# Kernel optimization log

Measured on AMD Instinct MI355X. Metric: run time of the kernel, lower is better.

## Reference

```python
import jax, jax.numpy as jnp
import numpy as np

B, NPG, EPG = 128, 256, 2048   # graphs, nodes/graph, edges/graph
EMB, EH, L = 256, 64, 5
ATOM_V, BOND_V = 119, 16


def setup_inputs() -> dict:
    key = jax.random.key(0)
    ks = iter(jax.random.split(key, 32))
    s = 0.02
    inp = {
        'atom_idx': jax.random.randint(next(ks), (B, NPG), 0, ATOM_V),
        'local_edge_index': jax.random.randint(next(ks), (B, 2, EPG), 0, NPG),
        'edge_attr_idx': jax.random.randint(next(ks), (B, EPG), 0, BOND_V),
        'order': 3,
        'atom_emb': jax.random.normal(next(ks), (ATOM_V, EMB), jnp.float32) * s,
        'bond_emb_h': jax.random.normal(next(ks), (BOND_V, EH), jnp.float32) * s,
        'edge_lin_w': jax.random.normal(next(ks), (EH,), jnp.float32) * s,
        'edge_lin_b': jax.random.normal(next(ks), (1,), jnp.float32) * s,
        'bond_emb_l': jax.random.normal(next(ks), (L, BOND_V, EMB), jnp.float32) * s,
        'gin_eps': jnp.zeros((L,), jnp.float32),
        'mlp_w1': jax.random.normal(next(ks), (L, EMB, 2 * EMB), jnp.float32) * s,
        'mlp_b1': jax.random.normal(next(ks), (L, 2 * EMB), jnp.float32) * s,
        'mlp_bn_g': jnp.ones((L, 2 * EMB), jnp.float32),
        'mlp_bn_b': jnp.zeros((L, 2 * EMB), jnp.float32),
        'mlp_w2': jax.random.normal(next(ks), (L, 2 * EMB, EMB), jnp.float32) * s,
        'mlp_b2': jax.random.normal(next(ks), (L, EMB), jnp.float32) * s,
        'out_bn_g': jnp.ones((L, EMB), jnp.float32),
        'out_bn_b': jnp.zeros((L, EMB), jnp.float32),
        'vn_emb': jnp.zeros((1, EMB), jnp.float32),  # init constant 0 as in source
        'vn_w1': jax.random.normal(next(ks), (L - 1, EMB, 2 * EMB), jnp.float32) * s,
        'vn_b1': jax.random.normal(next(ks), (L - 1, 2 * EMB), jnp.float32) * s,
        'vn_w2': jax.random.normal(next(ks), (L - 1, 2 * EMB, EMB), jnp.float32) * s,
        'vn_b2': jax.random.normal(next(ks), (L - 1, EMB), jnp.float32) * s,
    }
    return inp


def _batchnorm(x, g, b):
    # training-mode BN math (biased variance), eps=1e-5 as in torch.nn.BatchNorm1d
    mu = x.mean(0)
    var = ((x - mu) ** 2).mean(0)
    return (x - mu) * jax.lax.rsqrt(var + 1e-5) * g + b


def reference(atom_idx, local_edge_index, edge_attr_idx, order,
              atom_emb, bond_emb_h, edge_lin_w, edge_lin_b, bond_emb_l, gin_eps,
              mlp_w1, mlp_b1, mlp_bn_g, mlp_bn_b, mlp_w2, mlp_b2,
              out_bn_g, out_bn_b, vn_emb, vn_w1, vn_b1, vn_w2, vn_b2):
    Bg, n = atom_idx.shape
    emb = atom_emb.shape[1]
    N = Bg * n
    nl = gin_eps.shape[0]

    # ---- per-graph learned-adjacency dense propagation (adj_learn=1) ----
    fea = atom_emb[atom_idx]                                       # [B,n,emb]
    ew = jax.nn.sigmoid(jnp.einsum('beh,h->be', bond_emb_h[edge_attr_idx], edge_lin_w)
                        + edge_lin_b[0])                           # [B,e]

    def per_graph(f, ei, w):
        adj = jnp.zeros((n, n), f.dtype).at[ei[0], ei[1]].set(w)
        adj = adj + jnp.eye(n, dtype=f.dtype)
        # A = diag(colsum^-1/2) @ adj @ diag(rowsum^-1/2)  (as in source naming)
        r_row = adj.sum(0) ** -0.5
        r_col = adj.sum(1) ** -0.5
        A = r_row[:, None] * adj * r_col[None, :]
        x = f
        y = f
        for _ in range(order):
            x = A @ x
            y = y + x
        return y / (order + 1.0)

    h = jax.vmap(per_graph)(fea, local_edge_index, ew).reshape(N, emb)

    # ---- flatten batched graph to global edge list ----
    batch = jnp.repeat(jnp.arange(Bg), n)                          # [N]
    off = (jnp.arange(Bg) * n)[:, None]
    src = (local_edge_index[:, 0] + off).reshape(-1)               # [E]
    dst = (local_edge_index[:, 1] + off).reshape(-1)
    ea = edge_attr_idx.reshape(-1)

    # ---- virtual-node GIN stack (eval: dropout = identity) ----
    vn = jnp.broadcast_to(vn_emb[0], (Bg, emb))
    for l in range(nl):
        h = h + vn[batch]
        h_in = h
        eemb = bond_emb_l[l][ea]                                   # [E,emb]
        msg = jax.nn.relu(h[src] + eemb)
        agg = jax.ops.segment_sum(msg, dst, num_segments=N)
        z = (1.0 + gin_eps[l]) * h + agg
        z = _batchnorm(z @ mlp_w1[l] + mlp_b1[l], mlp_bn_g[l], mlp_bn_b[l])
        z = jax.nn.relu(z) @ mlp_w2[l] + mlp_b2[l]
        z = _batchnorm(z, out_bn_g[l], out_bn_b[l])
        if l < nl - 1:
            z = jax.nn.relu(z)
            vt = jax.ops.segment_sum(h_in, batch, num_segments=Bg) + vn
            vn = jax.nn.relu(jax.nn.relu(vt @ vn_w1[l] + vn_b1[l]) @ vn_w2[l] + vn_b2[l])
        h = z
    return h  # JK='last'
```

## Files before the change

kernel.cpp:

```cpp
#include <hip/hip_runtime.h>
#include <math.h>


#define B_G   128
#define NPG   256
#define EPG   2048
#define EMB   256
#define NL    5
#define NNODE (B_G*NPG)
#define NEDGE (B_G*EPG)
#define FBUF  8388608

typedef __attribute__((ext_vector_type(8))) short bf16x8;
typedef __attribute__((ext_vector_type(4))) float f32x4;

__device__ __forceinline__ void split1(float x, unsigned short& h, unsigned short& l) {
  unsigned u = __builtin_bit_cast(unsigned, x);
  unsigned hr = u + 0x7FFFu + ((u >> 16) & 1u);
  h = (unsigned short)(hr >> 16);
  float hf = __builtin_bit_cast(float, hr & 0xFFFF0000u);
  float r = x - hf;
  unsigned v = __builtin_bit_cast(unsigned, r);
  unsigned lr = v + 0x7FFFu + ((v >> 16) & 1u);
  l = (unsigned short)(lr >> 16);
}

__device__ __forceinline__ unsigned short round1(float x) {
  unsigned u = __builtin_bit_cast(unsigned, x);
  return (unsigned short)((u + 0x7FFFu + ((u >> 16) & 1u)) >> 16);
}

__device__ __forceinline__ float bdec(unsigned short h) {
  return __builtin_bit_cast(float, (unsigned)h << 16);
}

__device__ __forceinline__ void gload16(unsigned short* lds, const unsigned short* g) {
  __builtin_amdgcn_global_load_lds(
      (const __attribute__((address_space(1))) unsigned int*)g,
      (__attribute__((address_space(3))) unsigned int*)lds, 16, 0, 0);
}

__global__ void k_zero(uint4* p, int n16) {
  int i = blockIdx.x * 256 + threadIdx.x;
  if (i < n16) p[i] = make_uint4(0, 0, 0, 0);
}

__global__ void k_ewtbl(const float* __restrict__ bh, const float* __restrict__ w,
                        const float* __restrict__ b, float* __restrict__ tbl) {
  int v = threadIdx.x >> 6, t = threadIdx.x & 63;
  float p = bh[v * 64 + t] * w[t];
  for (int off = 32; off; off >>= 1) p += __shfl_down(p, off, 64);
  if (t == 0) tbl[v] = 1.0f / (1.0f + expf(-(p + b[0])));
}

__global__ void k_pack_adj(const int* __restrict__ lei, const int* __restrict__ ea,
                           int* __restrict__ packed) {
  int idx = blockIdx.x * 256 + threadIdx.x;
  int g = idx >> 11, e = idx & 2047;
  int s = lei[g * 4096 + e];
  int d = lei[g * 4096 + 2048 + e];
  int v = ((e + 1) << 4) | ea[g * 2048 + e];
  atomicMax(&packed[g * 65536 + s * 256 + d], v);
}

__global__ void k_unpack_adj(const int* __restrict__ packed,
                             const float* __restrict__ tbl, float* __restrict__ adj) {
  int idx = blockIdx.x * 256 + threadIdx.x;
  int v = packed[idx];
  adj[idx] = v ? tbl[v & 15] : 0.0f;
}

__global__ void k_addeye(float* __restrict__ adj) {
  int idx = blockIdx.x * 256 + threadIdx.x;
  int g = idx >> 8, i = idx & 255;
  adj[g * 65536 + i * 257] += 1.0f;
}

__global__ __launch_bounds__(256)
void k_degnorm(float* __restrict__ adj) {
  int g = blockIdx.x, t = threadIdx.x;
  float* Ag = adj + (size_t)g * 65536;
  __shared__ float cs[256];
  float s0 = 0, s1 = 0, s2 = 0, s3 = 0;
  for (int i = 0; i < 256; i += 4) {
    s0 += Ag[(i + 0) * 256 + t]; s1 += Ag[(i + 1) * 256 + t];
    s2 += Ag[(i + 2) * 256 + t]; s3 += Ag[(i + 3) * 256 + t];
  }
  cs[t] = rsqrtf((s0 + s1) + (s2 + s3));
  float4 r0 = make_float4(0, 0, 0, 0), r1 = r0, r2 = r0, r3 = r0;
  const float4* A4 = (const float4*)(Ag + t * 256);
  for (int j = 0; j < 64; j += 4) {
    float4 v0 = A4[j], v1 = A4[j + 1], v2 = A4[j + 2], v3 = A4[j + 3];
    r0.x += v0.x + v0.y; r0.y += v0.z + v0.w;
    r1.x += v1.x + v1.y; r1.y += v1.z + v1.w;
    r2.x += v2.x + v2.y; r2.y += v2.z + v2.w;
    r3.x += v3.x + v3.y; r3.y += v3.z + v3.w;
  }
  float rc = rsqrtf((r0.x + r0.y) + (r1.x + r1.y) + (r2.x + r2.y) + (r3.x + r3.y));
  __syncthreads();
  for (int i = 0; i < 256; i++) Ag[i * 256 + t] = cs[i] * Ag[i * 256 + t] * rc;
}

__global__ void k_feaT(const int* __restrict__ aidx, const float* __restrict__ aemb,
                       float* __restrict__ X0t, float* __restrict__ Yt) {
  int i = blockIdx.x * 256 + threadIdx.x;
  int g = i >> 16, e = (i >> 8) & 255, n = i & 255;
  int av = aidx[g * 256 + n];
  float v = aemb[av * 256 + e];
  X0t[i] = v; Yt[i] = v;
}

__global__ __launch_bounds__(256)
void k_transp(const float* __restrict__ src, float* __restrict__ dst,
              int K, int N, long ss, long sd, float scale) {
  __shared__ float tl[64][65];
  src += (size_t)blockIdx.z * ss; dst += (size_t)blockIdx.z * sd;
  int n0 = blockIdx.x * 64, k0 = blockIdx.y * 64;
  int t = threadIdx.x;
  int c = (t & 15) * 4, r = t >> 4;
#pragma unroll
  for (int p = 0; p < 4; p++) {
    int rr = r + p * 16;
    float4 v = *(const float4*)&src[(size_t)(k0 + rr) * N + n0 + c];
    tl[rr][c] = v.x; tl[rr][c + 1] = v.y; tl[rr][c + 2] = v.z; tl[rr][c + 3] = v.w;
  }
  __syncthreads();
#pragma unroll
  for (int p = 0; p < 4; p++) {
    int rr = r + p * 16;
    float4 o;
    o.x = tl[c][rr] * scale;     o.y = tl[c + 1][rr] * scale;
    o.z = tl[c + 2][rr] * scale; o.w = tl[c + 3][rr] * scale;
    *(float4*)&dst[(size_t)(n0 + rr) * K + k0 + c] = o;
  }
}

__global__ __launch_bounds__(256)
void k_wtsplit(const float* __restrict__ src, unsigned short* __restrict__ dh,
               unsigned short* __restrict__ dl, int K, int N, long ss, long sd) {
  __shared__ float tl[64][65];
  src += (size_t)blockIdx.z * ss;
  dh += (size_t)blockIdx.z * sd; dl += (size_t)blockIdx.z * sd;
  int n0 = blockIdx.x * 64, k0 = blockIdx.y * 64;
  int t = threadIdx.x;
  int c = (t & 15) * 4, r = t >> 4;
#pragma unroll
  for (int p = 0; p < 4; p++) {
    int rr = r + p * 16;
    float4 v = *(const float4*)&src[(size_t)(k0 + rr) * N + n0 + c];
    tl[rr][c] = v.x; tl[rr][c + 1] = v.y; tl[rr][c + 2] = v.z; tl[rr][c + 3] = v.w;
  }
  __syncthreads();
#pragma unroll
  for (int p = 0; p < 4; p++) {
    int rr = r + p * 16;
    ushort4 hh, ll;
    split1(tl[c][rr],     hh.x, ll.x);
    split1(tl[c + 1][rr], hh.y, ll.y);
    split1(tl[c + 2][rr], hh.z, ll.z);
    split1(tl[c + 3][rr], hh.w, ll.w);
    size_t o = (size_t)(n0 + rr) * K + k0 + c;
    *(ushort4*)&dh[o] = hh; *(ushort4*)&dl[o] = ll;
  }
}

__global__ __launch_bounds__(256, 2)
void k_mgemm(const float* __restrict__ A, const float* __restrict__ Bt,
             float* __restrict__ C, float* __restrict__ Yacc, int K, int N,
             long sA, long sBt, long sC) {
  __shared__ alignas(16) unsigned short Ah[128 * 64], Al[128 * 64];
  __shared__ alignas(16) unsigned short Bh[128 * 64], Bl[128 * 64];
  int z = blockIdx.z;
  A += (size_t)z * sA; Bt += (size_t)z * sBt; C += (size_t)z * sC;
  float* Yp = Yacc ? Yacc + (size_t)z * sC : nullptr;
  int rowbase = blockIdx.y * 128, colbase = blockIdx.x * 128;
  int t = threadIdx.x, l = t & 63, w = t >> 6;
  int wr = w >> 1, wc = w & 1;
  f32x4 acc[4][4];
#pragma unroll
  for (int i = 0; i < 4; i++)
#pragma unroll
    for (int j = 0; j < 4; j++) acc[i][j] = (f32x4){0, 0, 0, 0};

  for (int k0 = 0; k0 < K; k0 += 64) {
    __syncthreads();
    for (int p = 0; p < 8; p++) {
      int flat = p * 256 + t;
      int r = flat >> 4, kq = (flat & 15) * 4;
      float4 va = *(const float4*)&A[(size_t)(rowbase + r) * K + k0 + kq];
      int off = ((r * 128 + kq * 2) ^ ((r & 7) << 4)) >> 1;
      ushort4 hh, ll;
      split1(va.x, hh.x, ll.x); split1(va.y, hh.y, ll.y);
      split1(va.z, hh.z, ll.z); split1(va.w, hh.w, ll.w);
      *(ushort4*)&Ah[off] = hh; *(ushort4*)&Al[off] = ll;
      float4 vb = *(const float4*)&Bt[(size_t)(colbase + r) * K + k0 + kq];
      split1(vb.x, hh.x, ll.x); split1(vb.y, hh.y, ll.y);
      split1(vb.z, hh.z, ll.z); split1(vb.w, hh.w, ll.w);
      *(ushort4*)&Bh[off] = hh; *(ushort4*)&Bl[off] = ll;
    }
    __syncthreads();
#pragma unroll
    for (int ks = 0; ks < 2; ks++) {
      bf16x8 ah[4], al_[4], bh[4], bl[4];
#pragma unroll
      for (int fm = 0; fm < 4; fm++) {
        int r = wr * 64 + fm * 16 + (l & 15);
        int off = (r * 64 + ks * 32 + (l >> 4) * 8) ^ ((r & 7) << 3);
        ah[fm] = *(const bf16x8*)&Ah[off];
        al_[fm] = *(const bf16x8*)&Al[off];
      }
#pragma unroll
      for (int fn = 0; fn < 4; fn++) {
        int c = wc * 64 + fn * 16 + (l & 15);
        int off = (c * 64 + ks * 32 + (l >> 4) * 8) ^ ((c & 7) << 3);
        bh[fn] = *(const bf16x8*)&Bh[off];
        bl[fn] = *(const bf16x8*)&Bl[off];
      }
#pragma unroll
      for (int fm = 0; fm < 4; fm++)
#pragma unroll
        for (int fn = 0; fn < 4; fn++) {
          acc[fm][fn] = __builtin_amdgcn_mfma_f32_16x16x32_bf16(ah[fm], bh[fn], acc[fm][fn], 0, 0, 0);
          acc[fm][fn] = __builtin_amdgcn_mfma_f32_16x16x32_bf16(ah[fm], bl[fn], acc[fm][fn], 0, 0, 0);
          acc[fm][fn] = __builtin_amdgcn_mfma_f32_16x16x32_bf16(al_[fm], bh[fn], acc[fm][fn], 0, 0, 0);
        }
    }
  }
#pragma unroll
  for (int fm = 0; fm < 4; fm++)
#pragma unroll
    for (int r4 = 0; r4 < 4; r4++) {
      int row = rowbase + wr * 64 + fm * 16 + (l >> 4) * 4 + r4;
#pragma unroll
      for (int fn = 0; fn < 4; fn++) {
        int col = colbase + wc * 64 + fn * 16 + (l & 15);
        float v = acc[fm][fn][r4];
        size_t idx = (size_t)row * N + col;
        if (Yp) Yp[idx] += v;
        C[idx] = v;
      }
    }
}

__global__ __launch_bounds__(256, 4)
void k_bgemm(const unsigned short* __restrict__ A_g, const unsigned short* __restrict__ B_g,
             const float* __restrict__ bias, float* __restrict__ Cf,
             unsigned short* __restrict__ Ch,
             float* __restrict__ Ssum, float* __restrict__ Ssq, int K, int N) {
  __shared__ alignas(16) unsigned short As[128 * 64];
  __shared__ alignas(16) unsigned short Bs[128 * 64];
  int rowbase = blockIdx.y * 128, colbase = blockIdx.x * 128;
  int t = threadIdx.x, l = t & 63, wid = t >> 6;
  int wr = wid >> 1, wc = wid & 1;
  int r8 = l >> 3, cb = (l & 7) * 8;
  f32x4 acc[4][4];
#pragma unroll
  for (int i = 0; i < 4; i++)
#pragma unroll
    for (int j = 0; j < 4; j++) acc[i][j] = (f32x4){0, 0, 0, 0};

  for (int k0 = 0; k0 < K; k0 += 64) {
    __syncthreads();
#pragma unroll
    for (int i = 0; i < 4; i++) {
      int chunk = wid * 4 + i;
      int row = chunk * 8 + r8;
      gload16(As + chunk * 512, A_g + (size_t)(rowbase + row) * K + k0 + cb);
      gload16(Bs + chunk * 512, B_g + (size_t)(colbase + row) * K + k0 + cb);
    }
    __syncthreads();
#pragma unroll
    for (int ks = 0; ks < 2; ks++) {
      bf16x8 ah[4], bh[4];
#pragma unroll
      for (int fm = 0; fm < 4; fm++) {
        int r = wr * 64 + fm * 16 + (l & 15);
        ah[fm] = *(const bf16x8*)&As[r * 64 + ks * 32 + (l >> 4) * 8];
      }
#pragma unroll
      for (int fn = 0; fn < 4; fn++) {
        int c = wc * 64 + fn * 16 + (l & 15);
        bh[fn] = *(const bf16x8*)&Bs[c * 64 + ks * 32 + (l >> 4) * 8];
      }
#pragma unroll
      for (int fm = 0; fm < 4; fm++)
#pragma unroll
        for (int fn = 0; fn < 4; fn++)
          acc[fm][fn] = __builtin_amdgcn_mfma_f32_16x16x32_bf16(ah[fm], bh[fn], acc[fm][fn], 0, 0, 0);
    }
  }
  __syncthreads();
  float bi[4], scoll[4] = {0, 0, 0, 0}, qcoll[4] = {0, 0, 0, 0};
#pragma unroll
  for (int fn = 0; fn < 4; fn++)
    bi[fn] = bias ? bias[colbase + wc * 64 + fn * 16 + (l & 15)] : 0.0f;
#pragma unroll
  for (int fm = 0; fm < 4; fm++)
#pragma unroll
    for (int r4 = 0; r4 < 4; r4++) {
      int row = rowbase + wr * 64 + fm * 16 + (l >> 4) * 4 + r4;
#pragma unroll
      for (int fn = 0; fn < 4; fn++) {
        int col = colbase + wc * 64 + fn * 16 + (l & 15);
        float v = acc[fm][fn][r4] + bi[fn];
        size_t idx = (size_t)row * N + col;
        if (Cf) Cf[idx] = v;
        if (Ch) Ch[idx] = round1(v);
        scoll[fn] += v; qcoll[fn] += v * v;
      }
    }
  if (Ssum) {
    float* scr = (float*)As;
    scr[t] = 0.0f;
    __syncthreads();
#pragma unroll
    for (int fn = 0; fn < 4; fn++) {
      int cl_ = wc * 64 + fn * 16 + (l & 15);
      atomicAdd(&scr[cl_ * 2], scoll[fn]);
      atomicAdd(&scr[cl_ * 2 + 1], qcoll[fn]);
    }
    __syncthreads();
    if (t < 128) {
      atomicAdd(&Ssum[colbase + t], scr[t * 2]);
      atomicAdd(&Ssq[colbase + t], scr[t * 2 + 1]);
    }
  }
}

__global__ void k_bnsplit(unsigned short* __restrict__ Th,
                          const float* __restrict__ Ssum, const float* __restrict__ Ssq,
                          const float* __restrict__ g, const float* __restrict__ b) {
  size_t i = (size_t)blockIdx.x * 256 + threadIdx.x;
  int c4 = ((int)i & 127) * 4;
  ushort4 h4 = *(ushort4*)&Th[i * 4];
  float4 ss = *(const float4*)&Ssum[c4], qq = *(const float4*)&Ssq[c4];
  float4 gg = *(const float4*)&g[c4],    bb = *(const float4*)&b[c4];
  const float invN = 1.0f / 32768.0f;
  float x, mu, var, sc, sh;
#define BNS(cmp) \
  mu = ss.cmp * invN; var = qq.cmp * invN - mu * mu; \
  sc = rsqrtf(var + 1e-5f) * gg.cmp; sh = bb.cmp - mu * sc; \
  x = bdec(h4.cmp); x = fmaf(x, sc, sh); x = x > 0 ? x : 0; \
  h4.cmp = round1(x);
  BNS(x) BNS(y) BNS(z) BNS(w)
#undef BNS
  *(ushort4*)&Th[i * 4] = h4;
}

__global__ void k_count(const int* __restrict__ lei, int* __restrict__ counts) {
  int idx = blockIdx.x * 256 + threadIdx.x;
  int g = idx >> 11, e = idx & 2047;
  int d = lei[g * 4096 + 2048 + e];
  atomicAdd(&counts[g * 256 + d], 1);
}

__global__ void k_scan(const int* __restrict__ counts, int* __restrict__ rowptr,
                       int* __restrict__ pos) {
  int g = blockIdx.x, t = threadIdx.x;
  __shared__ int sc[256];
  int own = counts[g * 256 + t];
  sc[t] = own;
  __syncthreads();
  for (int off = 1; off < 256; off <<= 1) {
    int v = 0;
    if (t >= off) v = sc[t - off];
    __syncthreads();
    sc[t] += v;
    __syncthreads();
  }
  int val = g * 2048 + sc[t] - own;
  rowptr[g * 256 + t] = val;
  pos[g * 256 + t] = val;
  if (g == B_G - 1 && t == 255) rowptr[B_G * 256] = B_G * 2048;
}

__global__ void k_fill(const int* __restrict__ lei, const int* __restrict__ ea,
                       int* __restrict__ pos, int* __restrict__ csr) {
  int idx = blockIdx.x * 256 + threadIdx.x;
  int g = idx >> 11, e = idx & 2047;
  int s = lei[g * 4096 + e];
  int d = lei[g * 4096 + 2048 + e];
  int eav = ea[g * 2048 + e];
  int slot = atomicAdd(&pos[g * 256 + d], 1);
  csr[slot] = s | (eav << 16);
}

__global__ __launch_bounds__(256)
void k_agg(const float* __restrict__ H,
           const float* __restrict__ hsc, const float* __restrict__ hsh,
           const float* __restrict__ vn, int vns,
           const float* __restrict__ eemb,
           const int* __restrict__ rowptr, const int* __restrict__ csr,
           const float* __restrict__ geps, int l,
           unsigned short* __restrict__ Zh) {
  __shared__ float ee[16 * 256];
  for (int i = threadIdx.x; i < 4096; i += 256) ee[i] = eemb[i];
  __syncthreads();
  int lane = threadIdx.x & 63, w = threadIdx.x >> 6;
  int m = blockIdx.x * 4 + w;
  int g = m >> 8;
  int d = lane * 4;
  float eps1 = 1.0f + geps[l];
  float4 sc4 = make_float4(0, 0, 0, 0), sh4 = make_float4(0, 0, 0, 0);
  if (hsc) { sc4 = *(const float4*)&hsc[d]; sh4 = *(const float4*)&hsh[d]; }
  float4 vn4 = *(const float4*)&vn[(size_t)g * vns + d];
  int rp = rowptr[m], rp1 = rowptr[m + 1];
  float4 acc = make_float4(0, 0, 0, 0);
  int gbase = g << 8;
  for (int j = rp; j < rp1; j++) {
    int cw = csr[j];
    int src = cw & 0xFFFF, eav = cw >> 16;
    float4 h4 = *(const float4*)&H[(size_t)(gbase + src) * 256 + d];
    if (hsc) {
      h4.x = fmaf(h4.x, sc4.x, sh4.x); h4.y = fmaf(h4.y, sc4.y, sh4.y);
      h4.z = fmaf(h4.z, sc4.z, sh4.z); h4.w = fmaf(h4.w, sc4.w, sh4.w);
      h4.x = h4.x > 0 ? h4.x : 0; h4.y = h4.y > 0 ? h4.y : 0;
      h4.z = h4.z > 0 ? h4.z : 0; h4.w = h4.w > 0 ? h4.w : 0;
    }
    const float4 e4 = *(const float4*)&ee[eav * 256 + d];
    float mx = h4.x + vn4.x + e4.x; float my = h4.y + vn4.y + e4.y;
    float mz = h4.z + vn4.z + e4.z; float mw = h4.w + vn4.w + e4.w;
    acc.x += mx > 0 ? mx : 0; acc.y += my > 0 ? my : 0;
    acc.z += mz > 0 ? mz : 0; acc.w += mw > 0 ? mw : 0;
  }
  float4 hs = *(const float4*)&H[(size_t)m * 256 + d];
  if (hsc) {
    hs.x = fmaf(hs.x, sc4.x, sh4.x); hs.y = fmaf(hs.y, sc4.y, sh4.y);
    hs.z = fmaf(hs.z, sc4.z, sh4.z); hs.w = fmaf(hs.w, sc4.w, sh4.w);
    hs.x = hs.x > 0 ? hs.x : 0; hs.y = hs.y > 0 ? hs.y : 0;
    hs.z = hs.z > 0 ? hs.z : 0; hs.w = hs.w > 0 ? hs.w : 0;
  }
  float4 z4;
  z4.x = eps1 * (hs.x + vn4.x) + acc.x;
  z4.y = eps1 * (hs.y + vn4.y) + acc.y;
  z4.z = eps1 * (hs.z + vn4.z) + acc.z;
  z4.w = eps1 * (hs.w + vn4.w) + acc.w;
  ushort4 hh;
  hh.x = round1(z4.x); hh.y = round1(z4.y);
  hh.z = round1(z4.z); hh.w = round1(z4.w);
  *(ushort4*)&Zh[(size_t)m * 256 + d] = hh;
}

__global__ __launch_bounds__(256)
void k_vnsum(const float* __restrict__ H,
             const float* __restrict__ hsc, const float* __restrict__ hsh,
             float* __restrict__ VNP) {
  int g = blockIdx.x >> 1, p = blockIdx.x & 1, t = threadIdx.x;
  float sc = 0, sh = 0;
  if (hsc) { sc = hsc[t]; sh = hsh[t]; }
  int base = g * 256 + p * 128;
  float s0 = 0, s1 = 0, s2 = 0, s3 = 0;
  for (int i = 0; i < 128; i += 4) {
    float v0 = H[(size_t)(base + i + 0) * 256 + t];
    float v1 = H[(size_t)(base + i + 1) * 256 + t];
    float v2 = H[(size_t)(base + i + 2) * 256 + t];
    float v3 = H[(size_t)(base + i + 3) * 256 + t];
    if (hsc) {
      v0 = fmaf(v0, sc, sh); v0 = v0 > 0 ? v0 : 0;
      v1 = fmaf(v1, sc, sh); v1 = v1 > 0 ? v1 : 0;
      v2 = fmaf(v2, sc, sh); v2 = v2 > 0 ? v2 : 0;
      v3 = fmaf(v3, sc, sh); v3 = v3 > 0 ? v3 : 0;
    }
    s0 += v0; s1 += v1; s2 += v2; s3 += v3;
  }
  VNP[(size_t)(p * 128 + g) * 256 + t] = (s0 + s1) + (s2 + s3);
}

__global__ __launch_bounds__(256)
void k_vn(const float* __restrict__ VNP,
          const float* __restrict__ vn_in, int vns,
          const float* __restrict__ W1, const float* __restrict__ B1,
          const float* __restrict__ W2, const float* __restrict__ B2,
          float* __restrict__ vn_out) {
  int g = blockIdx.x, t = threadIdx.x;
  __shared__ float vt[256];
  __shared__ float u[512];
  vt[t] = VNP[(size_t)g * 256 + t] + VNP[(size_t)(128 + g) * 256 + t]
        + 257.0f * vn_in[(size_t)g * vns + t];
  __syncthreads();
  for (int o = t; o < 512; o += 256) {
    float a = B1[o];
    for (int k = 0; k < 256; k++) a = fmaf(vt[k], W1[k * 512 + o], a);
    u[o] = a > 0 ? a : 0;
  }
  __syncthreads();
  float a = B2[t];
  for (int k = 0; k < 512; k++) a = fmaf(u[k], W2[k * 256 + t], a);
  vn_out[g * 256 + t] = a > 0 ? a : 0;
}

__global__ void k_bnfin(const float* __restrict__ Ssum, const float* __restrict__ Ssq,
                        const float* __restrict__ g, const float* __restrict__ b,
                        float* __restrict__ scale, float* __restrict__ shift,
                        int NC, float invN) {
  int c = blockIdx.x * 256 + threadIdx.x;
  if (c >= NC) return;
  float mu = Ssum[c] * invN;
  float var = Ssq[c] * invN - mu * mu;
  float rs = rsqrtf(var + 1e-5f);
  float s = rs * g[c];
  scale[c] = s;
  shift[c] = b[c] - mu * s;
}

__global__ void k_final(const float* __restrict__ T2, const float* __restrict__ sc,
                        const float* __restrict__ sh, float* __restrict__ out) {
  int i = blockIdx.x * 256 + threadIdx.x;
  int c4 = (i & 63) * 4;
  float4 v = *(const float4*)&T2[(size_t)i * 4];
  float4 s4 = *(const float4*)&sc[c4];
  float4 h4 = *(const float4*)&sh[c4];
  v.x = fmaf(v.x, s4.x, h4.x); v.y = fmaf(v.y, s4.y, h4.y);
  v.z = fmaf(v.z, s4.z, h4.z); v.w = fmaf(v.w, s4.w, h4.w);
  *(float4*)&out[(size_t)i * 4] = v;
}

extern "C" void kernel_launch(void* const* d_in, const int* in_sizes, int n_in,
                              void* d_out, int out_size, void* d_ws, size_t ws_size,
                              hipStream_t stream) {
  (void)in_sizes; (void)n_in; (void)out_size; (void)ws_size;
  const int*   atom_idx = (const int*)d_in[0];
  const int*   lei      = (const int*)d_in[1];
  const int*   eattr    = (const int*)d_in[2];
  const float* atom_emb = (const float*)d_in[4];
  const float* bemb_h   = (const float*)d_in[5];
  const float* elw      = (const float*)d_in[6];
  const float* elb      = (const float*)d_in[7];
  const float* bemb_l   = (const float*)d_in[8];
  const float* geps     = (const float*)d_in[9];
  const float* mw1      = (const float*)d_in[10];
  const float* mb1      = (const float*)d_in[11];
  const float* mbng     = (const float*)d_in[12];
  const float* mbnb     = (const float*)d_in[13];
  const float* mw2      = (const float*)d_in[14];
  const float* mb2      = (const float*)d_in[15];
  const float* obng     = (const float*)d_in[16];
  const float* obnb     = (const float*)d_in[17];
  const float* vne      = (const float*)d_in[18];
  const float* vw1      = (const float*)d_in[19];
  const float* vb1      = (const float*)d_in[20];
  const float* vw2      = (const float*)d_in[21];
  const float* vb2      = (const float*)d_in[22];
  float* out = (float*)d_out;

  float* W   = (float*)d_ws;
  float* A_  = W;
  float* X0T = W + (size_t)FBUF;
  float* X1T = W + (size_t)2 * FBUF;
  float* YT  = W + (size_t)3 * FBUF;
  float* Z_  = W + (size_t)4 * FBUF;
  float* SM  = W + (size_t)5 * FBUF;
  float* EWT = SM;
  float* S1S = SM + 256;
  float* S1Q = SM + 768;
  float* S2S = SM + 1280;
  float* S2Q = SM + 1536;
  float* SC2 = SM + 1792;
  float* SH2 = SM + 2048;
  float* VNA = SM + 2304;
  float* VNB = SM + 35072;
  int* ROWPTR = (int*)(SM + 67840);
  int* POS    = ROWPTR + 32772;
  int* COUNTS = POS + 32768;
  int* CSR    = COUNTS + 32768;
  unsigned short* W1hT = (unsigned short*)(SM + 428544);
  unsigned short* W1lT = (unsigned short*)(SM + 756224);
  unsigned short* W2hT = (unsigned short*)(SM + 1083904);
  unsigned short* W2lT = (unsigned short*)(SM + 1411584);
  float* T2 = A_;
  float* H0 = X0T;
  unsigned short* T1h = (unsigned short*)X1T;
  unsigned short* Zh  = (unsigned short*)Z_;
  int* PACKED = (int*)Z_;
  float* VNP  = (float*)POS;

  k_zero<<<8192, 256, 0, stream>>>((uint4*)A_, 2097152);
  k_zero<<<8192, 256, 0, stream>>>((uint4*)PACKED, 2097152);
  k_zero<<<32, 256, 0, stream>>>((uint4*)COUNTS, 8192);
  k_ewtbl<<<1, 1024, 0, stream>>>(bemb_h, elw, elb, EWT);
  k_pack_adj<<<NEDGE / 256, 256, 0, stream>>>(lei, eattr, PACKED);
  k_unpack_adj<<<32768, 256, 0, stream>>>(PACKED, EWT, A_);
  k_addeye<<<NNODE / 256, 256, 0, stream>>>(A_);
  k_degnorm<<<B_G, 256, 0, stream>>>(A_);
  k_wtsplit<<<dim3(8, 4, 5), 256, 0, stream>>>(mw1, W1hT, W1lT, 256, 512, 131072, 131072);
  k_wtsplit<<<dim3(4, 8, 5), 256, 0, stream>>>(mw2, W2hT, W2lT, 512, 256, 131072, 131072);
  k_feaT<<<32768, 256, 0, stream>>>(atom_idx, atom_emb, X0T, YT);
  k_mgemm<<<dim3(2, 2, B_G), 256, 0, stream>>>(X0T, A_, X1T, YT, 256, 256, 65536, 65536, 65536);
  k_mgemm<<<dim3(2, 2, B_G), 256, 0, stream>>>(X1T, A_, X0T, YT, 256, 256, 65536, 65536, 65536);
  k_mgemm<<<dim3(2, 2, B_G), 256, 0, stream>>>(X0T, A_, X1T, YT, 256, 256, 65536, 65536, 65536);
  k_transp<<<dim3(4, 4, B_G), 256, 0, stream>>>(YT, H0, 256, 256, 65536, 65536, 0.25f);

  k_count<<<NEDGE / 256, 256, 0, stream>>>(lei, COUNTS);
  k_scan<<<B_G, 256, 0, stream>>>(COUNTS, ROWPTR, POS);
  k_fill<<<NEDGE / 256, 256, 0, stream>>>(lei, eattr, POS, CSR);

  const float* vn_cur = vne; int vns = 0;
  float* vn_next = VNA;
  for (int l = 0; l < NL; l++) {
    const float* hsrc = (l == 0) ? H0 : T2;
    const float* hsc  = (l == 0) ? nullptr : SC2;
    const float* hsh  = (l == 0) ? nullptr : SH2;
    k_agg<<<NNODE / 4, 256, 0, stream>>>(hsrc, hsc, hsh, vn_cur, vns,
        bemb_l + (size_t)l * 16 * EMB, ROWPTR, CSR, geps, l, Zh);
    if (l < NL - 1) {
      k_vnsum<<<256, 256, 0, stream>>>(hsrc, hsc, hsh, VNP);
      k_vn<<<B_G, 256, 0, stream>>>(VNP, vn_cur, vns,
          vw1 + (size_t)l * EMB * 512, vb1 + (size_t)l * 512,
          vw2 + (size_t)l * 512 * EMB, vb2 + (size_t)l * EMB, vn_next);
    }
    k_zero<<<2, 256, 0, stream>>>((uint4*)S1S, 384);
    k_bgemm<<<dim3(4, 256), 256, 0, stream>>>(Zh,
        W1hT + (size_t)l * 131072, mb1 + (size_t)l * 512,
        nullptr, T1h, S1S, S1Q, 256, 512);
    k_bnsplit<<<16384, 256, 0, stream>>>(T1h, S1S, S1Q,
        mbng + (size_t)l * 512, mbnb + (size_t)l * 512);
    k_bgemm<<<dim3(2, 256), 256, 0, stream>>>(T1h,
        W2hT + (size_t)l * 131072, mb2 + (size_t)l * 256,
        T2, nullptr, S2S, S2Q, 512, 256);
    k_bnfin<<<1, 256, 0, stream>>>(S2S, S2Q, obng + (size_t)l * EMB,
        obnb + (size_t)l * EMB, SC2, SH2, 256, 1.0f / NNODE);
    if (l < NL - 1) {
      vn_cur = vn_next; vns = EMB;
      vn_next = (vn_next == VNA) ? VNB : VNA;
    }
  }
  k_final<<<8192, 256, 0, stream>>>(T2, SC2, SH2, out);
}
```

Measured before the change: 1.197 ms.

## Replace split-bf16 propagation GEMMs with single-bf16 batched GEMMs

```diff
diff --git a/kernel.cpp b/kernel.cpp
--- a/kernel.cpp
+++ b/kernel.cpp
@@ -14,17 +14,6 @@
 typedef __attribute__((ext_vector_type(8))) short bf16x8;
 typedef __attribute__((ext_vector_type(4))) float f32x4;
 
-__device__ __forceinline__ void split1(float x, unsigned short& h, unsigned short& l) {
-  unsigned u = __builtin_bit_cast(unsigned, x);
-  unsigned hr = u + 0x7FFFu + ((u >> 16) & 1u);
-  h = (unsigned short)(hr >> 16);
-  float hf = __builtin_bit_cast(float, hr & 0xFFFF0000u);
-  float r = x - hf;
-  unsigned v = __builtin_bit_cast(unsigned, r);
-  unsigned lr = v + 0x7FFFu + ((v >> 16) & 1u);
-  l = (unsigned short)(lr >> 16);
-}
-
 __device__ __forceinline__ unsigned short round1(float x) {
   unsigned u = __builtin_bit_cast(unsigned, x);
   return (unsigned short)((u + 0x7FFFu + ((u >> 16) & 1u)) >> 16);
@@ -67,26 +56,21 @@
                              const float* __restrict__ tbl, float* __restrict__ adj) {
   int idx = blockIdx.x * 256 + threadIdx.x;
   int v = packed[idx];
-  adj[idx] = v ? tbl[v & 15] : 0.0f;
-}
-
-__global__ void k_addeye(float* __restrict__ adj) {
-  int idx = blockIdx.x * 256 + threadIdx.x;
-  int g = idx >> 8, i = idx & 255;
-  adj[g * 65536 + i * 257] += 1.0f;
+  int r = (idx >> 8) & 255, c = idx & 255;
+  adj[idx] = (v ? tbl[v & 15] : 0.0f) + (r == c ? 1.0f : 0.0f);
 }
 
 __global__ __launch_bounds__(256)
-void k_degnorm(float* __restrict__ adj) {
+void k_degsums(const float* __restrict__ adj, float* __restrict__ CSv,
+               float* __restrict__ RCv) {
   int g = blockIdx.x, t = threadIdx.x;
-  float* Ag = adj + (size_t)g * 65536;
-  __shared__ float cs[256];
+  const float* Ag = adj + (size_t)g * 65536;
   float s0 = 0, s1 = 0, s2 = 0, s3 = 0;
   for (int i = 0; i < 256; i += 4) {
     s0 += Ag[(i + 0) * 256 + t]; s1 += Ag[(i + 1) * 256 + t];
     s2 += Ag[(i + 2) * 256 + t]; s3 += Ag[(i + 3) * 256 + t];
   }
-  cs[t] = rsqrtf((s0 + s1) + (s2 + s3));
+  CSv[g * 256 + t] = rsqrtf((s0 + s1) + (s2 + s3));
   float4 r0 = make_float4(0, 0, 0, 0), r1 = r0, r2 = r0, r3 = r0;
   const float4* A4 = (const float4*)(Ag + t * 256);
   for (int j = 0; j < 64; j += 4) {
@@ -96,25 +80,77 @@
     r2.x += v2.x + v2.y; r2.y += v2.z + v2.w;
     r3.x += v3.x + v3.y; r3.y += v3.z + v3.w;
   }
-  float rc = rsqrtf((r0.x + r0.y) + (r1.x + r1.y) + (r2.x + r2.y) + (r3.x + r3.y));
-  __syncthreads();
-  for (int i = 0; i < 256; i++) Ag[i * 256 + t] = cs[i] * Ag[i * 256 + t] * rc;
-}
-
-__global__ void k_feaT(const int* __restrict__ aidx, const float* __restrict__ aemb,
-                       float* __restrict__ X0t, float* __restrict__ Yt) {
-  int i = blockIdx.x * 256 + threadIdx.x;
-  int g = i >> 16, e = (i >> 8) & 255, n = i & 255;
-  int av = aidx[g * 256 + n];
-  float v = aemb[av * 256 + e];
-  X0t[i] = v; Yt[i] = v;
+  RCv[g * 256 + t] = rsqrtf((r0.x + r0.y) + (r1.x + r1.y) + (r2.x + r2.y) + (r3.x + r3.y));
+}
+
+__global__ void k_ascale(const float* __restrict__ adj, const float* __restrict__ CSv,
+                         const float* __restrict__ RCv, unsigned short* __restrict__ Ahb) {
+  int flat = blockIdx.x * 256 + threadIdx.x;
+  int g = flat >> 14;
+  int i = (flat >> 6) & 255, j4 = (flat & 63) * 4;
+  size_t base = (size_t)g * 65536 + i * 256 + j4;
+  float4 a = *(const float4*)&adj[base];
+  float cs = CSv[g * 256 + i];
+  float4 rc = *(const float4*)&RCv[g * 256 + j4];
+  ushort4 o;
+  o.x = round1(cs * a.x * rc.x); o.y = round1(cs * a.y * rc.y);
+  o.z = round1(cs * a.z * rc.z); o.w = round1(cs * a.w * rc.w);
+  *(ushort4*)&Ahb[base] = o;
+}
+
+__global__ void k_feaTb(const int* __restrict__ aidx, const float* __restrict__ aemb,
+                        unsigned short* __restrict__ X0h) {
+  int flat = blockIdx.x * 256 + threadIdx.x;
+  int base = flat * 4;
+  int g = base >> 16, e = (base >> 8) & 255, n0 = base & 255;
+  const int* ai = &aidx[g * 256 + n0];
+  ushort4 o;
+  o.x = round1(aemb[ai[0] * 256 + e]);
+  o.y = round1(aemb[ai[1] * 256 + e]);
+  o.z = round1(aemb[ai[2] * 256 + e]);
+  o.w = round1(aemb[ai[3] * 256 + e]);
+  *(ushort4*)&X0h[base] = o;
 }
 
 __global__ __launch_bounds__(256)
-void k_transp(const float* __restrict__ src, float* __restrict__ dst,
-              int K, int N, long ss, long sd, float scale) {
+void k_sumT(const unsigned short* __restrict__ X0, const unsigned short* __restrict__ X1,
+            const unsigned short* __restrict__ X2, const unsigned short* __restrict__ X3,
+            float* __restrict__ dst) {
   __shared__ float tl[64][65];
-  src += (size_t)blockIdx.z * ss; dst += (size_t)blockIdx.z * sd;
+  size_t zo = (size_t)blockIdx.z * 65536;
+  int n0 = blockIdx.x * 64, k0 = blockIdx.y * 64;
+  int t = threadIdx.x;
+  int c = (t & 15) * 4, r = t >> 4;
+#pragma unroll
+  for (int p = 0; p < 4; p++) {
+    int rr = r + p * 16;
+    size_t off = zo + (size_t)(k0 + rr) * 256 + n0 + c;
+    ushort4 a = *(const ushort4*)&X0[off];
+    ushort4 b = *(const ushort4*)&X1[off];
+    ushort4 cc = *(const ushort4*)&X2[off];
+    ushort4 d = *(const ushort4*)&X3[off];
+    tl[rr][c + 0] = bdec(a.x) + bdec(b.x) + bdec(cc.x) + bdec(d.x);
+    tl[rr][c + 1] = bdec(a.y) + bdec(b.y) + bdec(cc.y) + bdec(d.y);
+    tl[rr][c + 2] = bdec(a.z) + bdec(b.z) + bdec(cc.z) + bdec(d.z);
+    tl[rr][c + 3] = bdec(a.w) + bdec(b.w) + bdec(cc.w) + bdec(d.w);
+  }
+  __syncthreads();
+#pragma unroll
+  for (int p = 0; p < 4; p++) {
+    int rr = r + p * 16;
+    float4 o;
+    o.x = tl[c][rr] * 0.25f;     o.y = tl[c + 1][rr] * 0.25f;
+    o.z = tl[c + 2][rr] * 0.25f; o.w = tl[c + 3][rr] * 0.25f;
+    *(float4*)&dst[zo + (size_t)(n0 + rr) * 256 + k0 + c] = o;
+  }
+}
+
+__global__ __launch_bounds__(256)
+void k_wtb(const float* __restrict__ src, unsigned short* __restrict__ dh,
+           int K, int N, long ss, long sd) {
+  __shared__ float tl[64][65];
+  src += (size_t)blockIdx.z * ss;
+  dh += (size_t)blockIdx.z * sd;
   int n0 = blockIdx.x * 64, k0 = blockIdx.y * 64;
   int t = threadIdx.x;
   int c = (t & 15) * 4, r = t >> 4;
@@ -128,127 +164,25 @@
 #pragma unroll
   for (int p = 0; p < 4; p++) {
     int rr = r + p * 16;
-    float4 o;
-    o.x = tl[c][rr] * scale;     o.y = tl[c + 1][rr] * scale;
-    o.z = tl[c + 2][rr] * scale; o.w = tl[c + 3][rr] * scale;
-    *(float4*)&dst[(size_t)(n0 + rr) * K + k0 + c] = o;
-  }
-}
-
-__global__ __launch_bounds__(256)
-void k_wtsplit(const float* __restrict__ src, unsigned short* __restrict__ dh,
-               unsigned short* __restrict__ dl, int K, int N, long ss, long sd) {
-  __shared__ float tl[64][65];
-  src += (size_t)blockIdx.z * ss;
-  dh += (size_t)blockIdx.z * sd; dl += (size_t)blockIdx.z * sd;
-  int n0 = blockIdx.x * 64, k0 = blockIdx.y * 64;
-  int t = threadIdx.x;
-  int c = (t & 15) * 4, r = t >> 4;
-#pragma unroll
-  for (int p = 0; p < 4; p++) {
-    int rr = r + p * 16;
-    float4 v = *(const float4*)&src[(size_t)(k0 + rr) * N + n0 + c];
-    tl[rr][c] = v.x; tl[rr][c + 1] = v.y; tl[rr][c + 2] = v.z; tl[rr][c + 3] = v.w;
-  }
-  __syncthreads();
-#pragma unroll
-  for (int p = 0; p < 4; p++) {
-    int rr = r + p * 16;
-    ushort4 hh, ll;
-    split1(tl[c][rr],     hh.x, ll.x);
-    split1(tl[c + 1][rr], hh.y, ll.y);
-    split1(tl[c + 2][rr], hh.z, ll.z);
-    split1(tl[c + 3][rr], hh.w, ll.w);
-    size_t o = (size_t)(n0 + rr) * K + k0 + c;
-    *(ushort4*)&dh[o] = hh; *(ushort4*)&dl[o] = ll;
-  }
-}
-
-__global__ __launch_bounds__(256, 2)
-void k_mgemm(const float* __restrict__ A, const float* __restrict__ Bt,
-             float* __restrict__ C, float* __restrict__ Yacc, int K, int N,
-             long sA, long sBt, long sC) {
-  __shared__ alignas(16) unsigned short Ah[128 * 64], Al[128 * 64];
-  __shared__ alignas(16) unsigned short Bh[128 * 64], Bl[128 * 64];
-  int z = blockIdx.z;
-  A += (size_t)z * sA; Bt += (size_t)z * sBt; C += (size_t)z * sC;
-  float* Yp = Yacc ? Yacc + (size_t)z * sC : nullptr;
-  int rowbase = blockIdx.y * 128, colbase = blockIdx.x * 128;
-  int t = threadIdx.x, l = t & 63, w = t >> 6;
-  int wr = w >> 1, wc = w & 1;
-  f32x4 acc[4][4];
-#pragma unroll
-  for (int i = 0; i < 4; i++)
-#pragma unroll
-    for (int j = 0; j < 4; j++) acc[i][j] = (f32x4){0, 0, 0, 0};
-
-  for (int k0 = 0; k0 < K; k0 += 64) {
-    __syncthreads();
-    for (int p = 0; p < 8; p++) {
-      int flat = p * 256 + t;
-      int r = flat >> 4, kq = (flat & 15) * 4;
-      float4 va = *(const float4*)&A[(size_t)(rowbase + r) * K + k0 + kq];
-      int off = ((r * 128 + kq * 2) ^ ((r & 7) << 4)) >> 1;
-      ushort4 hh, ll;
-      split1(va.x, hh.x, ll.x); split1(va.y, hh.y, ll.y);
-      split1(va.z, hh.z, ll.z); split1(va.w, hh.w, ll.w);
-      *(ushort4*)&Ah[off] = hh; *(ushort4*)&Al[off] = ll;
-      float4 vb = *(const float4*)&Bt[(size_t)(colbase + r) * K + k0 + kq];
-      split1(vb.x, hh.x, ll.x); split1(vb.y, hh.y, ll.y);
-      split1(vb.z, hh.z, ll.z); split1(vb.w, hh.w, ll.w);
-      *(ushort4*)&Bh[off] = hh; *(ushort4*)&Bl[off] = ll;
-    }
-    __syncthreads();
-#pragma unroll
-    for (int ks = 0; ks < 2; ks++) {
-      bf16x8 ah[4], al_[4], bh[4], bl[4];
-#pragma unroll
-      for (int fm = 0; fm < 4; fm++) {
-        int r = wr * 64 + fm * 16 + (l & 15);
-        int off = (r * 64 + ks * 32 + (l >> 4) * 8) ^ ((r & 7) << 3);
-        ah[fm] = *(const bf16x8*)&Ah[off];
-        al_[fm] = *(const bf16x8*)&Al[off];
-      }
-#pragma unroll
-      for (int fn = 0; fn < 4; fn++) {
-        int c = wc * 64 + fn * 16 + (l & 15);
-        int off = (c * 64 + ks * 32 + (l >> 4) * 8) ^ ((c & 7) << 3);
-        bh[fn] = *(const bf16x8*)&Bh[off];
-        bl[fn] = *(const bf16x8*)&Bl[off];
-      }
-#pragma unroll
-      for (int fm = 0; fm < 4; fm++)
-#pragma unroll
-        for (int fn = 0; fn < 4; fn++) {
-          acc[fm][fn] = __builtin_amdgcn_mfma_f32_16x16x32_bf16(ah[fm], bh[fn], acc[fm][fn], 0, 0, 0);
-          acc[fm][fn] = __builtin_amdgcn_mfma_f32_16x16x32_bf16(ah[fm], bl[fn], acc[fm][fn], 0, 0, 0);
-          acc[fm][fn] = __builtin_amdgcn_mfma_f32_16x16x32_bf16(al_[fm], bh[fn], acc[fm][fn], 0, 0, 0);
-        }
-    }
-  }
-#pragma unroll
-  for (int fm = 0; fm < 4; fm++)
-#pragma unroll
-    for (int r4 = 0; r4 < 4; r4++) {
-      int row = rowbase + wr * 64 + fm * 16 + (l >> 4) * 4 + r4;
-#pragma unroll
-      for (int fn = 0; fn < 4; fn++) {
-        int col = colbase + wc * 64 + fn * 16 + (l & 15);
-        float v = acc[fm][fn][r4];
-        size_t idx = (size_t)row * N + col;
-        if (Yp) Yp[idx] += v;
-        C[idx] = v;
-      }
-    }
+    ushort4 hh;
+    hh.x = round1(tl[c][rr]);     hh.y = round1(tl[c + 1][rr]);
+    hh.z = round1(tl[c + 2][rr]); hh.w = round1(tl[c + 3][rr]);
+    *(ushort4*)&dh[(size_t)(n0 + rr) * K + k0 + c] = hh;
+  }
 }
 
 __global__ __launch_bounds__(256, 4)
 void k_bgemm(const unsigned short* __restrict__ A_g, const unsigned short* __restrict__ B_g,
              const float* __restrict__ bias, float* __restrict__ Cf,
              unsigned short* __restrict__ Ch,
-             float* __restrict__ Ssum, float* __restrict__ Ssq, int K, int N) {
+             float* __restrict__ Ssum, float* __restrict__ Ssq, int K, int N,
+             long zA, long zB, long zC) {
   __shared__ alignas(16) unsigned short As[128 * 64];
   __shared__ alignas(16) unsigned short Bs[128 * 64];
+  int z = blockIdx.z;
+  A_g += (size_t)z * zA; B_g += (size_t)z * zB;
+  if (Cf) Cf += (size_t)z * zC;
+  if (Ch) Ch += (size_t)z * zC;
   int rowbase = blockIdx.y * 128, colbase = blockIdx.x * 128;
   int t = threadIdx.x, l = t & 63, wid = t >> 6;
   int wr = wid >> 1, wc = wid & 1;
@@ -545,9 +479,9 @@
 
   float* W   = (float*)d_ws;
   float* A_  = W;
-  float* X0T = W + (size_t)FBUF;
-  float* X1T = W + (size_t)2 * FBUF;
-  float* YT  = W + (size_t)3 * FBUF;
+  float* U1  = W + (size_t)FBUF;
+  float* U2  = W + (size_t)2 * FBUF;
+  float* U3  = W + (size_t)3 * FBUF;
   float* Z_  = W + (size_t)4 * FBUF;
   float* SM  = W + (size_t)5 * FBUF;
   float* EWT = SM;
@@ -559,36 +493,43 @@
   float* SH2 = SM + 2048;
   float* VNA = SM + 2304;
   float* VNB = SM + 35072;
-  int* ROWPTR = (int*)(SM + 67840);
+  float* CSv = SM + 67840;
+  float* RCv = SM + 100608;
+  int* ROWPTR = (int*)(SM + 133376);
   int* POS    = ROWPTR + 32772;
   int* COUNTS = POS + 32768;
   int* CSR    = COUNTS + 32768;
-  unsigned short* W1hT = (unsigned short*)(SM + 428544);
-  unsigned short* W1lT = (unsigned short*)(SM + 756224);
-  unsigned short* W2hT = (unsigned short*)(SM + 1083904);
-  unsigned short* W2lT = (unsigned short*)(SM + 1411584);
+  unsigned short* W1hT = (unsigned short*)(SM + 493952);
+  unsigned short* W2hT = (unsigned short*)(SM + 821632);
   float* T2 = A_;
-  float* H0 = X0T;
-  unsigned short* T1h = (unsigned short*)X1T;
+  float* H0 = U3;
+  int* PACKED = (int*)U3;
+  unsigned short* X0h = (unsigned short*)U1;
+  unsigned short* X1h = X0h + 8388608;
+  unsigned short* X2h = (unsigned short*)U2;
+  unsigned short* X3h = X2h + 8388608;
+  unsigned short* T1h = (unsigned short*)U1;
   unsigned short* Zh  = (unsigned short*)Z_;
-  int* PACKED = (int*)Z_;
+  unsigned short* Ahb = (unsigned short*)(Z_ + (size_t)FBUF / 2);
   float* VNP  = (float*)POS;
 
-  k_zero<<<8192, 256, 0, stream>>>((uint4*)A_, 2097152);
   k_zero<<<8192, 256, 0, stream>>>((uint4*)PACKED, 2097152);
   k_zero<<<32, 256, 0, stream>>>((uint4*)COUNTS, 8192);
   k_ewtbl<<<1, 1024, 0, stream>>>(bemb_h, elw, elb, EWT);
   k_pack_adj<<<NEDGE / 256, 256, 0, stream>>>(lei, eattr, PACKED);
   k_unpack_adj<<<32768, 256, 0, stream>>>(PACKED, EWT, A_);
-  k_addeye<<<NNODE / 256, 256, 0, stream>>>(A_);
-  k_degnorm<<<B_G, 256, 0, stream>>>(A_);
-  k_wtsplit<<<dim3(8, 4, 5), 256, 0, stream>>>(mw1, W1hT, W1lT, 256, 512, 131072, 131072);
-  k_wtsplit<<<dim3(4, 8, 5), 256, 0, stream>>>(mw2, W2hT, W2lT, 512, 256, 131072, 131072);
-  k_feaT<<<32768, 256, 0, stream>>>(atom_idx, atom_emb, X0T, YT);
-  k_mgemm<<<dim3(2, 2, B_G), 256, 0, stream>>>(X0T, A_, X1T, YT, 256, 256, 65536, 65536, 65536);
-  k_mgemm<<<dim3(2, 2, B_G), 256, 0, stream>>>(X1T, A_, X0T, YT, 256, 256, 65536, 65536, 65536);
-  k_mgemm<<<dim3(2, 2, B_G), 256, 0, stream>>>(X0T, A_, X1T, YT, 256, 256, 65536, 65536, 65536);
-  k_transp<<<dim3(4, 4, B_G), 256, 0, stream>>>(YT, H0, 256, 256, 65536, 65536, 0.25f);
+  k_degsums<<<B_G, 256, 0, stream>>>(A_, CSv, RCv);
+  k_ascale<<<8192, 256, 0, stream>>>(A_, CSv, RCv, Ahb);
+  k_wtb<<<dim3(8, 4, 5), 256, 0, stream>>>(mw1, W1hT, 256, 512, 131072, 131072);
+  k_wtb<<<dim3(4, 8, 5), 256, 0, stream>>>(mw2, W2hT, 512, 256, 131072, 131072);
+  k_feaTb<<<8192, 256, 0, stream>>>(atom_idx, atom_emb, X0h);
+  k_bgemm<<<dim3(2, 2, B_G), 256, 0, stream>>>(X0h, Ahb, nullptr, nullptr, X1h,
+      nullptr, nullptr, 256, 256, 65536, 65536, 65536);
+  k_bgemm<<<dim3(2, 2, B_G), 256, 0, stream>>>(X1h, Ahb, nullptr, nullptr, X2h,
+      nullptr, nullptr, 256, 256, 65536, 65536, 65536);
+  k_bgemm<<<dim3(2, 2, B_G), 256, 0, stream>>>(X2h, Ahb, nullptr, nullptr, X3h,
+      nullptr, nullptr, 256, 256, 65536, 65536, 65536);
+  k_sumT<<<dim3(4, 4, B_G), 256, 0, stream>>>(X0h, X1h, X2h, X3h, H0);
 
   k_count<<<NEDGE / 256, 256, 0, stream>>>(lei, COUNTS);
   k_scan<<<B_G, 256, 0, stream>>>(COUNTS, ROWPTR, POS);
@@ -609,14 +550,14 @@
           vw2 + (size_t)l * 512 * EMB, vb2 + (size_t)l * EMB, vn_next);
     }
     k_zero<<<2, 256, 0, stream>>>((uint4*)S1S, 384);
-    k_bgemm<<<dim3(4, 256), 256, 0, stream>>>(Zh,
+    k_bgemm<<<dim3(4, 256, 1), 256, 0, stream>>>(Zh,
         W1hT + (size_t)l * 131072, mb1 + (size_t)l * 512,
-        nullptr, T1h, S1S, S1Q, 256, 512);
+        nullptr, T1h, S1S, S1Q, 256, 512, 0, 0, 0);
     k_bnsplit<<<16384, 256, 0, stream>>>(T1h, S1S, S1Q,
         mbng + (size_t)l * 512, mbnb + (size_t)l * 512);
-    k_bgemm<<<dim3(2, 256), 256, 0, stream>>>(T1h,
+    k_bgemm<<<dim3(2, 256, 1), 256, 0, stream>>>(T1h,
         W2hT + (size_t)l * 131072, mb2 + (size_t)l * 256,
-        T2, nullptr, S2S, S2Q, 512, 256);
+        T2, nullptr, S2S, S2Q, 512, 256, 0, 0, 0);
     k_bnfin<<<1, 256, 0, stream>>>(S2S, S2Q, obng + (size_t)l * EMB,
         obnb + (size_t)l * EMB, SC2, SH2, 256, 1.0f / NNODE);
     if (l < NL - 1) {
```

Result: faster. 1.084 ms (-9.5%).
